# Performance work log

Hardware: AMD Instinct MI355X
Metric: run time of the kernel (lower is better)

The kernel has to match this reference:

```python
import jax, jax.numpy as jnp
import numpy as np

B, S, D, H, DFF = 8, 1024, 1024, 16, 4096
DK = D // H
EPS = 1e-5


def layernorm(x, g, b):
    mu = jnp.mean(x, axis=-1, keepdims=True)
    var = jnp.var(x, axis=-1, keepdims=True)
    return (x - mu) * jax.lax.rsqrt(var + EPS) * g + b


def mha(q_in, k_in, v_in, wq, bq, wk, bk, wv, bv, wo, bo):
    # weights stored as [in, out] (transposed torch Linear)
    nb = q_in.shape[0]
    def split(t):  # [B,S,D] -> [B,H,S,DK]
        return t.reshape(nb, -1, H, DK).transpose(0, 2, 1, 3)
    q = split(q_in @ wq + bq)
    k = split(k_in @ wk + bk)
    v = split(v_in @ wv + bv)
    scores = jnp.einsum('bhqd,bhkd->bhqk', q, k) / jnp.sqrt(jnp.float32(DK))
    p = jax.nn.softmax(scores, axis=-1)
    o = jnp.einsum('bhqk,bhkd->bhqd', p, v)
    o = o.transpose(0, 2, 1, 3).reshape(nb, -1, D)
    return o @ wo + bo


def setup_inputs() -> dict:
    key = jax.random.key(0)
    ks = jax.random.split(key, 40)
    i = iter(range(40))
    def rn(shape, scale=1.0):
        return jax.random.normal(ks[next(i)], shape, dtype=jnp.float32) * scale
    d = {}
    d['x'] = rn((B, S, D))
    d['y'] = rn((B, S, D))
    d['x_pos'] = rn((B, S, D))
    d['y_pos'] = rn((B, S, D))
    w_scale = 1.0 / np.sqrt(D)
    for pfx in ('sa', 'ca'):
        for nm in ('q', 'k', 'v', 'o'):
            d[f'{pfx}_w{nm}'] = rn((D, D), w_scale)
            d[f'{pfx}_b{nm}'] = jnp.zeros((D,), jnp.float32)
    d['ffn_w1'] = rn((D, DFF), w_scale)
    d['ffn_b1'] = jnp.zeros((DFF,), jnp.float32)
    d['ffn_w2'] = rn((DFF, D), 1.0 / np.sqrt(DFF))
    d['ffn_b2'] = jnp.zeros((D,), jnp.float32)
    for n in (1, 2, 3, 4):
        d[f'ln{n}_g'] = jnp.ones((D,), jnp.float32)
        d[f'ln{n}_b'] = jnp.zeros((D,), jnp.float32)
    return d


def reference(x, y, x_pos, y_pos,
              sa_wq, sa_bq, sa_wk, sa_bk, sa_wv, sa_bv, sa_wo, sa_bo,
              ca_wq, ca_bq, ca_wk, ca_bk, ca_wv, ca_bv, ca_wo, ca_bo,
              ffn_w1, ffn_b1, ffn_w2, ffn_b2,
              ln1_g, ln1_b, ln2_g, ln2_b, ln3_g, ln3_b, ln4_g, ln4_b):
    # pre-norm variant (norm_before=True), eval mode (dropout=0)
    x2 = layernorm(x, ln1_g, ln1_b)
    qk = x2 + x_pos
    x = x + mha(qk, qk, x2, sa_wq, sa_bq, sa_wk, sa_bk, sa_wv, sa_bv, sa_wo, sa_bo)
    x2 = layernorm(x, ln2_g, ln2_b)
    y2 = layernorm(y, ln3_g, ln3_b)
    x = x + mha(x2 + x_pos, y2 + y_pos, y2,
                ca_wq, ca_bq, ca_wk, ca_bk, ca_wv, ca_bv, ca_wo, ca_bo)
    x2 = layernorm(x, ln4_g, ln4_b)
    h = x2 @ ffn_w1 + ffn_b1
    h = h * jax.nn.sigmoid(h)  # Swish
    return x + (h @ ffn_w2 + ffn_b2)
```

## Files before the change

### kernel.cpp

```cpp
#include <hip/hip_runtime.h>
#include <hip/hip_bf16.h>

#define NB 8
#define NS 1024
#define ND 1024
#define NH 16
#define NDK 64
#define NDFF 4096

typedef __bf16 bf16;
typedef __attribute__((ext_vector_type(8))) __bf16 bf16x8;
typedef __attribute__((ext_vector_type(4))) __bf16 bf16x4;
typedef __attribute__((ext_vector_type(4))) float f32x4;

__device__ __forceinline__ void gload16(const bf16* g, bf16* l) {
  __builtin_amdgcn_global_load_lds(
      (const __attribute__((address_space(1))) void*)g,
      (__attribute__((address_space(3))) void*)l, 16, 0, 0);
}

__global__ void wconv_t(const float* __restrict__ W, bf16* __restrict__ WT,
                        int K, int N) {
  __shared__ float tile[32][33];
  int n0 = blockIdx.x * 32, k0 = blockIdx.y * 32;
  int tx = threadIdx.x, ty = threadIdx.y;
#pragma unroll
  for (int i2 = 0; i2 < 4; ++i2) {
    int i = ty + i2 * 8;
    tile[i][tx] = W[(long)(k0 + i) * N + n0 + tx];
  }
  __syncthreads();
#pragma unroll
  for (int i2 = 0; i2 < 4; ++i2) {
    int i = ty + i2 * 8;
    WT[(long)(n0 + i) * K + k0 + tx] = (bf16)tile[tx][i];
  }
}

__global__ void ln_fused(const float* __restrict__ in, const float* __restrict__ gam,
                         const float* __restrict__ bet, const float* __restrict__ pos,
                         bf16* __restrict__ out_ln, bf16* __restrict__ out_lnpos) {
  long row = blockIdx.x;
  int t = threadIdx.x;
  float4 v = ((const float4*)(in + row * ND))[t];
  float s = v.x + v.y + v.z + v.w;
  float s2 = v.x * v.x + v.y * v.y + v.z * v.z + v.w * v.w;
#pragma unroll
  for (int m = 32; m >= 1; m >>= 1) {
    s += __shfl_xor(s, m);
    s2 += __shfl_xor(s2, m);
  }
  __shared__ float red[8];
  if ((t & 63) == 0) {
    red[t >> 6] = s;
    red[4 + (t >> 6)] = s2;
  }
  __syncthreads();
  float ts = red[0] + red[1] + red[2] + red[3];
  float ts2 = red[4] + red[5] + red[6] + red[7];
  float mu = ts * (1.0f / ND);
  float var = ts2 * (1.0f / ND) - mu * mu;
  float rstd = rsqrtf(var + 1e-5f);
  float4 g4 = ((const float4*)gam)[t];
  float4 b4 = ((const float4*)bet)[t];
  float o0 = (v.x - mu) * rstd * g4.x + b4.x;
  float o1 = (v.y - mu) * rstd * g4.y + b4.y;
  float o2 = (v.z - mu) * rstd * g4.z + b4.z;
  float o3 = (v.w - mu) * rstd * g4.w + b4.w;
  if (out_ln) {
    bf16x4 q;
    q[0] = (bf16)o0; q[1] = (bf16)o1; q[2] = (bf16)o2; q[3] = (bf16)o3;
    *(bf16x4*)(out_ln + row * ND + t * 4) = q;
  }
  if (out_lnpos) {
    float4 p4 = ((const float4*)(pos + row * ND))[t];
    bf16x4 q;
    q[0] = (bf16)(o0 + p4.x); q[1] = (bf16)(o1 + p4.y);
    q[2] = (bf16)(o2 + p4.z); q[3] = (bf16)(o3 + p4.w);
    *(bf16x4*)(out_lnpos + row * ND + t * 4) = q;
  }
}

template <int MODE>
__global__ __launch_bounds__(512) void gemm_bt(
    const bf16* __restrict__ A, const bf16* __restrict__ WT,
    const float* __restrict__ bias, const float* __restrict__ res,
    void* __restrict__ out, int M, int N, int K) {
  __shared__ bf16 SA[3][256 * 64];
  __shared__ bf16 SB[3][128 * 64];
  const int t = threadIdx.x;
  const int w = t >> 6, l = t & 63;
  const int wr = w >> 1, wc = w & 1;
  const int c = l & 15, g = l >> 4, c7 = l & 7;
  const long row0 = (long)blockIdx.x * 256;
  const long col0 = (long)blockIdx.y * 128;
  const int NT = K >> 6;

  f32x4 acc[4][4];
#pragma unroll
  for (int m = 0; m < 4; ++m)
#pragma unroll
    for (int n = 0; n < 4; ++n) acc[m][n] = (f32x4){0.f, 0.f, 0.f, 0.f};

  const int lr = l >> 3;
  const int lu8 = ((l & 7) ^ lr) * 8;
  const bf16* Ag = A + (row0 + lr) * (long)K + lu8;
  const bf16* Bg = WT + (col0 + lr) * (long)K + lu8;

#define STG(PTR, SM, BS, RB, K0) \
  gload16((PTR) + (long)(RB) * K + (K0), &SM[BS][(RB)*64])
#define STAGE_H1(BS, K0)                \
  do {                                  \
    STG(Ag, SA, BS, w * 8, K0);         \
    STG(Ag, SA, BS, 64 + w * 8, K0);    \
    STG(Bg, SB, BS, w * 8, K0);         \
  } while (0)
#define STAGE_H2(BS, K0)                \
  do {                                  \
    STG(Ag, SA, BS, 128 + w * 8, K0);   \
    STG(Ag, SA, BS, 192 + w * 8, K0);   \
    STG(Bg, SB, BS, 64 + w * 8, K0);    \
  } while (0)

  STAGE_H1(0, 0);
  STAGE_H2(0, 0);
  STAGE_H1(1, 64);
  STAGE_H2(1, 64);

  for (int tt = 0; tt < NT; ++tt) {
    const int bc = tt % 3;
    const int bs = (tt + 2) % 3;
    const int kst = (tt + 2) << 6;
    const bool st = (tt + 2) < NT;
    if (tt + 1 < NT) {
      asm volatile("s_waitcnt vmcnt(6)" ::: "memory");
    } else {
      asm volatile("s_waitcnt vmcnt(0)" ::: "memory");
    }
    __syncthreads();
#pragma unroll
    for (int ks = 0; ks < 2; ++ks) {
      bf16x8 af[4], bfr[4];
#pragma unroll
      for (int m = 0; m < 4; ++m)
        af[m] = *(const bf16x8*)((const char*)SA[bc] +
                 ((wr * 64 + m * 16 + c) * 128 + (((ks << 2) + g) ^ c7) * 16));
#pragma unroll
      for (int n = 0; n < 4; ++n)
        bfr[n] = *(const bf16x8*)((const char*)SB[bc] +
                 ((wc * 64 + n * 16 + c) * 128 + (((ks << 2) + g) ^ c7) * 16));
      if (st) {
        if (ks == 0) STAGE_H1(bs, kst);
        else STAGE_H2(bs, kst);
      }
      __builtin_amdgcn_s_barrier();
      asm volatile("s_waitcnt lgkmcnt(0)" ::: "memory");
      __builtin_amdgcn_sched_barrier(0);
      __builtin_amdgcn_s_setprio(1);
#pragma unroll
      for (int m = 0; m < 4; ++m)
#pragma unroll
        for (int n = 0; n < 4; ++n)
          acc[m][n] = __builtin_amdgcn_mfma_f32_16x16x32_bf16(af[m], bfr[n], acc[m][n], 0, 0, 0);
      __builtin_amdgcn_s_setprio(0);
      __builtin_amdgcn_s_barrier();
    }
  }
#undef STG
#undef STAGE_H1
#undef STAGE_H2

#pragma unroll
  for (int n = 0; n < 4; ++n) {
    const long col = col0 + wc * 64 + n * 16 + c;
    const float bv = bias[col];
#pragma unroll
    for (int m = 0; m < 4; ++m) {
      const long rowb = row0 + wr * 64 + m * 16 + g * 4;
#pragma unroll
      for (int r = 0; r < 4; ++r) {
        float v = acc[m][n][r] + bv;
        const long idx = (rowb + r) * N + col;
        if (MODE == 0) {
          ((bf16*)out)[idx] = (bf16)v;
        } else if (MODE == 1) {
          ((float*)out)[idx] = res[idx] + v;
        } else {
          float sw = v / (1.f + __expf(-v));
          ((bf16*)out)[idx] = (bf16)sw;
        }
      }
    }
  }
}

__global__ void vtrans(const bf16* __restrict__ V, bf16* __restrict__ VT) {
  __shared__ bf16 tile[32][33];
  int st = blockIdx.x * 32, dt = blockIdx.y * 32;
  int bh = blockIdx.z;
  int b = bh >> 4, h = bh & 15;
  int tx = threadIdx.x, ty = threadIdx.y;
#pragma unroll
  for (int i2 = 0; i2 < 4; ++i2) {
    int i = ty + i2 * 8;
    tile[i][tx] = V[((long)b * NS + st + i) * ND + h * NDK + dt + tx];
  }
  __syncthreads();
#pragma unroll
  for (int i2 = 0; i2 < 4; ++i2) {
    int i = ty + i2 * 8;
    VT[((long)bh * NDK + dt + i) * NS + st + tx] = tile[tx][i];
  }
}

__global__ __launch_bounds__(256) void attn_fwd(
    const bf16* __restrict__ Q, const bf16* __restrict__ Kt,
    const bf16* __restrict__ VT, bf16* __restrict__ O) {
  __shared__ bf16 Ks[2][64 * 64];
  __shared__ bf16 Vs[2][64 * 64];
  __shared__ bf16 Pl[4][2][16 * 68];
  int t = threadIdx.x;
  int w = t >> 6, l = t & 63;
  int c = l & 15, g = l >> 4;
  int bid = blockIdx.x;
  int qt = bid >> 7, bh = bid & 127;
  int b = bh >> 4, h = bh & 15;
  int q0 = qt * 128 + w * 32;
  int swz = (c & 7) << 4;

  bf16x8 qf[2][2];
  const bf16* Qbase = Q + (long)(b * NS) * ND + h * NDK;
#pragma unroll
  for (int sj = 0; sj < 2; ++sj) {
    const bf16* qr = Qbase + (long)(q0 + sj * 16 + c) * ND + g * 8;
    qf[sj][0] = *(const bf16x8*)qr;
    qf[sj][1] = *(const bf16x8*)(qr + 32);
  }

  const bf16* Kg = Kt + (long)(b * NS) * ND + h * NDK;
  const bf16* Vg = VT + (long)(b * NH + h) * NDK * NS;

  int sr = l >> 3;
  int sc8 = 8 * ((l & 7) ^ sr);

  f32x4 o[2][4];
#pragma unroll
  for (int sj = 0; sj < 2; ++sj)
#pragma unroll
    for (int ds = 0; ds < 4; ++ds) o[sj][ds] = (f32x4){0.f, 0.f, 0.f, 0.f};
  float mx[2] = {-1e30f, -1e30f};
  float lsum[2] = {0.f, 0.f};

#define STAGE(BUF, KV)                                                        \
  {                                                                           \
    _Pragma("unroll") for (int j = 0; j < 2; ++j) {                           \
      int row = w * 16 + j * 8 + sr;                                          \
      gload16(Kg + (long)((KV) + row) * ND + sc8,                             \
              &Ks[BUF][(w * 16 + j * 8) * 64]);                               \
      gload16(Vg + (long)row * NS + (KV) + sc8,                               \
              &Vs[BUF][(w * 16 + j * 8) * 64]);                               \
    }                                                                         \
  }

  STAGE(0, 0);
  asm volatile("s_waitcnt vmcnt(0)" ::: "memory");
  __syncthreads();

  int buf = 0;
  for (int it = 0; it < NS / 64; ++it) {
    if (it + 1 < NS / 64) STAGE(buf ^ 1, (it + 1) * 64);

    f32x4 sv[2][4];
#pragma unroll
    for (int sj = 0; sj < 2; ++sj)
#pragma unroll
      for (int kt = 0; kt < 4; ++kt) sv[sj][kt] = (f32x4){0.f, 0.f, 0.f, 0.f};
    __builtin_amdgcn_s_setprio(1);
#pragma unroll
    for (int kt = 0; kt < 4; ++kt) {
      const char* kr = (const char*)&Ks[buf][(kt * 16 + c) * 64];
      bf16x8 ka0 = *(const bf16x8*)(kr + ((g * 16) ^ swz));
      bf16x8 ka1 = *(const bf16x8*)(kr + ((64 + g * 16) ^ swz));
#pragma unroll
      for (int sj = 0; sj < 2; ++sj) {
        sv[sj][kt] = __builtin_amdgcn_mfma_f32_16x16x32_bf16(ka0, qf[sj][0], sv[sj][kt], 0, 0, 0);
        sv[sj][kt] = __builtin_amdgcn_mfma_f32_16x16x32_bf16(ka1, qf[sj][1], sv[sj][kt], 0, 0, 0);
      }
    }
    __builtin_amdgcn_s_setprio(0);

    float pm[2];
#pragma unroll
    for (int sj = 0; sj < 2; ++sj) {
      float m = -1e30f;
#pragma unroll
      for (int kt = 0; kt < 4; ++kt)
#pragma unroll
        for (int r = 0; r < 4; ++r) {
          sv[sj][kt][r] *= 0.125f;
          m = fmaxf(m, sv[sj][kt][r]);
        }
      m = fmaxf(m, __shfl_xor(m, 16));
      m = fmaxf(m, __shfl_xor(m, 32));
      pm[sj] = m;
    }
    int cond = (pm[0] <= mx[0] + 8.f) && (pm[1] <= mx[1] + 8.f);
    if (!__all(cond)) {
#pragma unroll
      for (int sj = 0; sj < 2; ++sj) {
        float mn = fmaxf(mx[sj], pm[sj]);
        float sc = __expf(mx[sj] - mn);
        mx[sj] = mn;
        lsum[sj] *= sc;
#pragma unroll
        for (int ds = 0; ds < 4; ++ds)
#pragma unroll
          for (int r = 0; r < 4; ++r) o[sj][ds][r] *= sc;
      }
    }
#pragma unroll
    for (int sj = 0; sj < 2; ++sj) {
      float rs = 0.f;
#pragma unroll
      for (int kt = 0; kt < 4; ++kt) {
        bf16x4 pw;
#pragma unroll
        for (int r = 0; r < 4; ++r) {
          float e = __expf(sv[sj][kt][r] - mx[sj]);
          rs += e;
          pw[r] = (bf16)e;
        }
        *(bf16x4*)&Pl[w][sj][c * 68 + kt * 16 + 4 * g] = pw;
      }
      rs += __shfl_xor(rs, 16);
      rs += __shfl_xor(rs, 32);
      lsum[sj] += rs;
    }
    asm volatile("s_waitcnt lgkmcnt(0)" ::: "memory");
    __builtin_amdgcn_sched_barrier(0);

    __builtin_amdgcn_s_setprio(1);
#pragma unroll
    for (int ks = 0; ks < 2; ++ks) {
      bf16x8 pb0 = *(const bf16x8*)&Pl[w][0][c * 68 + ks * 32 + g * 8];
      bf16x8 pb1 = *(const bf16x8*)&Pl[w][1][c * 68 + ks * 32 + g * 8];
#pragma unroll
      for (int ds = 0; ds < 4; ++ds) {
        const char* vr = (const char*)&Vs[buf][(ds * 16 + c) * 64];
        bf16x8 va = *(const bf16x8*)(vr + ((ks * 64 + g * 16) ^ swz));
        o[0][ds] = __builtin_amdgcn_mfma_f32_16x16x32_bf16(va, pb0, o[0][ds], 0, 0, 0);
        o[1][ds] = __builtin_amdgcn_mfma_f32_16x16x32_bf16(va, pb1, o[1][ds], 0, 0, 0);
      }
    }
    __builtin_amdgcn_s_setprio(0);
    __syncthreads();
    buf ^= 1;
  }

#pragma unroll
  for (int sj = 0; sj < 2; ++sj) {
    float inv = 1.f / lsum[sj];
    bf16* Orow = O + (long)(b * NS + q0 + sj * 16 + c) * ND + h * NDK;
#pragma unroll
    for (int ds = 0; ds < 4; ++ds) {
      bf16x4 ov;
#pragma unroll
      for (int r = 0; r < 4; ++r) ov[r] = (bf16)(o[sj][ds][r] * inv);
      *(bf16x4*)(Orow + ds * 16 + 4 * g) = ov;
    }
  }
#undef STAGE
}

extern "C" void kernel_launch(void* const* d_in, const int* in_sizes, int n_in,
                              void* d_out, int out_size, void* d_ws, size_t ws_size,
                              hipStream_t stream) {
  (void)in_sizes; (void)n_in; (void)out_size; (void)ws_size;
  const float* x = (const float*)d_in[0];
  const float* y = (const float*)d_in[1];
  const float* x_pos = (const float*)d_in[2];
  const float* y_pos = (const float*)d_in[3];

  char* ws = (char*)d_ws;
  const size_t MB = 1ull << 20;
  bf16* Wt[8];
  for (int i = 0; i < 8; ++i) Wt[i] = (bf16*)(ws + (size_t)i * 2 * MB);
  bf16* W1T = (bf16*)(ws + 16 * MB);
  bf16* W2T = (bf16*)(ws + 24 * MB);
  float* xres = (float*)(ws + 32 * MB);
  bf16* x2 = (bf16*)(ws + 64 * MB);
  bf16* qk = (bf16*)(ws + 80 * MB);
  bf16* y2 = (bf16*)(ws + 96 * MB);
  bf16* yk = (bf16*)(ws + 112 * MB);
  bf16* Qb = (bf16*)(ws + 128 * MB);
  bf16* Kb = (bf16*)(ws + 144 * MB);
  bf16* Vb = (bf16*)(ws + 160 * MB);
  bf16* VTb = (bf16*)(ws + 176 * MB);
  bf16* Ob = (bf16*)(ws + 192 * MB);
  bf16* hb = (bf16*)(ws + 128 * MB);

  dim3 tb(32, 8);
  for (int i = 0; i < 8; ++i)
    wconv_t<<<dim3(32, 32), tb, 0, stream>>>((const float*)d_in[4 + 2 * i], Wt[i], 1024, 1024);
  wconv_t<<<dim3(128, 32), tb, 0, stream>>>((const float*)d_in[20], W1T, 1024, 4096);
  wconv_t<<<dim3(32, 128), tb, 0, stream>>>((const float*)d_in[22], W2T, 4096, 1024);

  const float* ln1g = (const float*)d_in[24]; const float* ln1b = (const float*)d_in[25];
  const float* ln2g = (const float*)d_in[26]; const float* ln2b = (const float*)d_in[27];
  const float* ln3g = (const float*)d_in[28]; const float* ln3b = (const float*)d_in[29];
  const float* ln4g = (const float*)d_in[30]; const float* ln4b = (const float*)d_in[31];

  dim3 gD(32, 8);
  dim3 gF1(32, 32);
  dim3 gVT(32, 2, 128);

  ln_fused<<<8192, 256, 0, stream>>>(x, ln1g, ln1b, x_pos, x2, qk);
  gemm_bt<0><<<gD, 512, 0, stream>>>(qk, Wt[0], (const float*)d_in[5], nullptr, Qb, 8192, 1024, 1024);
  gemm_bt<0><<<gD, 512, 0, stream>>>(qk, Wt[1], (const float*)d_in[7], nullptr, Kb, 8192, 1024, 1024);
  gemm_bt<0><<<gD, 512, 0, stream>>>(x2, Wt[2], (const float*)d_in[9], nullptr, Vb, 8192, 1024, 1024);
  vtrans<<<gVT, tb, 0, stream>>>(Vb, VTb);
  attn_fwd<<<1024, 256, 0, stream>>>(Qb, Kb, VTb, Ob);
  gemm_bt<1><<<gD, 512, 0, stream>>>(Ob, Wt[3], (const float*)d_in[11], x, xres, 8192, 1024, 1024);

  ln_fused<<<8192, 256, 0, stream>>>(xres, ln2g, ln2b, x_pos, nullptr, qk);
  ln_fused<<<8192, 256, 0, stream>>>(y, ln3g, ln3b, y_pos, y2, yk);
  gemm_bt<0><<<gD, 512, 0, stream>>>(qk, Wt[4], (const float*)d_in[13], nullptr, Qb, 8192, 1024, 1024);
  gemm_bt<0><<<gD, 512, 0, stream>>>(yk, Wt[5], (const float*)d_in[15], nullptr, Kb, 8192, 1024, 1024);
  gemm_bt<0><<<gD, 512, 0, stream>>>(y2, Wt[6], (const float*)d_in[17], nullptr, Vb, 8192, 1024, 1024);
  vtrans<<<gVT, tb, 0, stream>>>(Vb, VTb);
  attn_fwd<<<1024, 256, 0, stream>>>(Qb, Kb, VTb, Ob);
  gemm_bt<1><<<gD, 512, 0, stream>>>(Ob, Wt[7], (const float*)d_in[19], xres, xres, 8192, 1024, 1024);

  ln_fused<<<8192, 256, 0, stream>>>(xres, ln4g, ln4b, nullptr, x2, nullptr);
  gemm_bt<2><<<gF1, 512, 0, stream>>>(x2, W1T, (const float*)d_in[21], nullptr, hb, 8192, 4096, 1024);
  gemm_bt<1><<<gD, 512, 0, stream>>>(hb, W2T, (const float*)d_in[23], xres, (float*)d_out, 8192, 1024, 4096);
}
```

Measured before the change: 720.7 us.

## Restructure GEMM pipeline to 5-stage K=32 buffering with two blocks per CU

The bf16 GEMM now stages 32-wide K slices instead of 64 and keeps five LDS buffers instead of three, so four tiles are in flight ahead of compute. The LDS swizzle and load mapping are rebuilt for the narrower tiles, and each iteration uses one barrier pair instead of two sub-steps. LDS use drops from 144KB to 120KB and launch bounds ask for two blocks per CU, aiming for more memory-latency hiding. In exchange the loop does half as much MFMA work per barrier, and register pressure may rise under the occupancy hint.

```diff
diff --git a/kernel.cpp b/kernel.cpp
--- a/kernel.cpp
+++ b/kernel.cpp
@@ -82,19 +82,21 @@
 }
 
 template <int MODE>
-__global__ __launch_bounds__(512) void gemm_bt(
+__global__ __launch_bounds__(512, 2) void gemm_bt(
     const bf16* __restrict__ A, const bf16* __restrict__ WT,
     const float* __restrict__ bias, const float* __restrict__ res,
     void* __restrict__ out, int M, int N, int K) {
-  __shared__ bf16 SA[3][256 * 64];
-  __shared__ bf16 SB[3][128 * 64];
+  __shared__ bf16 SA[5][256 * 32];
+  __shared__ bf16 SB[5][128 * 32];
   const int t = threadIdx.x;
   const int w = t >> 6, l = t & 63;
-  const int wr = w >> 1, wc = w & 1;
-  const int c = l & 15, g = l >> 4, c7 = l & 7;
+  const int wr = w >> 2, wc = w & 3;
+  const int wrm = w >> 1, wcn = w & 1;
+  (void)wr; (void)wc;
+  const int c = l & 15, g = l >> 4;
   const long row0 = (long)blockIdx.x * 256;
   const long col0 = (long)blockIdx.y * 128;
-  const int NT = K >> 6;
+  const int NT = K >> 5;
 
   f32x4 acc[4][4];
 #pragma unroll
@@ -102,81 +104,78 @@
 #pragma unroll
     for (int n = 0; n < 4; ++n) acc[m][n] = (f32x4){0.f, 0.f, 0.f, 0.f};
 
-  const int lr = l >> 3;
-  const int lu8 = ((l & 7) ^ lr) * 8;
-  const bf16* Ag = A + (row0 + lr) * (long)K + lu8;
-  const bf16* Bg = WT + (col0 + lr) * (long)K + lu8;
-
-#define STG(PTR, SM, BS, RB, K0) \
-  gload16((PTR) + (long)(RB) * K + (K0), &SM[BS][(RB)*64])
-#define STAGE_H1(BS, K0)                \
-  do {                                  \
-    STG(Ag, SA, BS, w * 8, K0);         \
-    STG(Ag, SA, BS, 64 + w * 8, K0);    \
-    STG(Bg, SB, BS, w * 8, K0);         \
+  const int lr = l >> 2;
+  const int lcol = 8 * ((l & 3) ^ ((l >> 3) & 3));
+  const bf16* Ag0 = A + (row0 + w * 32 + lr) * (long)K + lcol;
+  const bf16* Ag1 = Ag0 + 16 * (long)K;
+  const bf16* Bg0 = WT + (col0 + w * 16 + lr) * (long)K + lcol;
+
+#define STAGE(BS, KK)                              \
+  do {                                             \
+    gload16(Ag0 + (KK), &SA[BS][(w * 32) * 32]);   \
+    gload16(Ag1 + (KK), &SA[BS][(w * 32 + 16) * 32]); \
+    gload16(Bg0 + (KK), &SB[BS][(w * 16) * 32]);   \
   } while (0)
-#define STAGE_H2(BS, K0)                \
-  do {                                  \
-    STG(Ag, SA, BS, 128 + w * 8, K0);   \
-    STG(Ag, SA, BS, 192 + w * 8, K0);   \
-    STG(Bg, SB, BS, 64 + w * 8, K0);    \
-  } while (0)
-
-  STAGE_H1(0, 0);
-  STAGE_H2(0, 0);
-  STAGE_H1(1, 64);
-  STAGE_H2(1, 64);
-
+
+  STAGE(0, 0);
+  STAGE(1, 32);
+  STAGE(2, 64);
+  STAGE(3, 96);
+
+  const int swz8 = (g ^ ((c >> 1) & 3)) * 8;
+  int aoff[4], boff[4];
+#pragma unroll
+  for (int m = 0; m < 4; ++m) aoff[m] = (wrm * 64 + m * 16 + c) * 32 + swz8;
+#pragma unroll
+  for (int n = 0; n < 4; ++n) boff[n] = (wcn * 64 + n * 16 + c) * 32 + swz8;
+
+  int cb = 0, sb = 4;
+  int ks_off = 128;
   for (int tt = 0; tt < NT; ++tt) {
-    const int bc = tt % 3;
-    const int bs = (tt + 2) % 3;
-    const int kst = (tt + 2) << 6;
-    const bool st = (tt + 2) < NT;
-    if (tt + 1 < NT) {
+    const int rem = NT - 1 - tt;
+    if (rem >= 3) {
+      asm volatile("s_waitcnt vmcnt(9)" ::: "memory");
+    } else if (rem == 2) {
       asm volatile("s_waitcnt vmcnt(6)" ::: "memory");
+    } else if (rem == 1) {
+      asm volatile("s_waitcnt vmcnt(3)" ::: "memory");
     } else {
       asm volatile("s_waitcnt vmcnt(0)" ::: "memory");
     }
-    __syncthreads();
-#pragma unroll
-    for (int ks = 0; ks < 2; ++ks) {
-      bf16x8 af[4], bfr[4];
-#pragma unroll
-      for (int m = 0; m < 4; ++m)
-        af[m] = *(const bf16x8*)((const char*)SA[bc] +
-                 ((wr * 64 + m * 16 + c) * 128 + (((ks << 2) + g) ^ c7) * 16));
+    __builtin_amdgcn_s_barrier();
+
+    const int ca = cb * (256 * 32);
+    const int cbb = cb * (128 * 32);
+    bf16x8 af[4], bfr[4];
+#pragma unroll
+    for (int m = 0; m < 4; ++m) af[m] = *(const bf16x8*)&SA[0][ca + aoff[m]];
+#pragma unroll
+    for (int n = 0; n < 4; ++n) bfr[n] = *(const bf16x8*)&SB[0][cbb + boff[n]];
+
+    if (tt + 4 < NT) STAGE(sb, ks_off);
+
+    __builtin_amdgcn_s_barrier();
+    __builtin_amdgcn_s_setprio(1);
+#pragma unroll
+    for (int m = 0; m < 4; ++m)
 #pragma unroll
       for (int n = 0; n < 4; ++n)
-        bfr[n] = *(const bf16x8*)((const char*)SB[bc] +
-                 ((wc * 64 + n * 16 + c) * 128 + (((ks << 2) + g) ^ c7) * 16));
-      if (st) {
-        if (ks == 0) STAGE_H1(bs, kst);
-        else STAGE_H2(bs, kst);
-      }
-      __builtin_amdgcn_s_barrier();
-      asm volatile("s_waitcnt lgkmcnt(0)" ::: "memory");
-      __builtin_amdgcn_sched_barrier(0);
-      __builtin_amdgcn_s_setprio(1);
-#pragma unroll
-      for (int m = 0; m < 4; ++m)
-#pragma unroll
-        for (int n = 0; n < 4; ++n)
-          acc[m][n] = __builtin_amdgcn_mfma_f32_16x16x32_bf16(af[m], bfr[n], acc[m][n], 0, 0, 0);
-      __builtin_amdgcn_s_setprio(0);
-      __builtin_amdgcn_s_barrier();
-    }
-  }
-#undef STG
-#undef STAGE_H1
-#undef STAGE_H2
+        acc[m][n] = __builtin_amdgcn_mfma_f32_16x16x32_bf16(af[m], bfr[n], acc[m][n], 0, 0, 0);
+    __builtin_amdgcn_s_setprio(0);
+
+    cb = (cb == 4) ? 0 : cb + 1;
+    sb = (sb == 4) ? 0 : sb + 1;
+    ks_off += 32;
+  }
+#undef STAGE
 
 #pragma unroll
   for (int n = 0; n < 4; ++n) {
-    const long col = col0 + wc * 64 + n * 16 + c;
+    const long col = col0 + wcn * 64 + n * 16 + c;
     const float bv = bias[col];
 #pragma unroll
     for (int m = 0; m < 4; ++m) {
-      const long rowb = row0 + wr * 64 + m * 16 + g * 4;
+      const long rowb = row0 + wrm * 64 + m * 16 + g * 4;
 #pragma unroll
       for (int r = 0; r < 4; ++r) {
         float v = acc[m][n][r] + bv;
```

New measurement: 698.8 us. 3.0% less time.
